# Optimization experiments

Hardware: AMD Instinct MI355X
Metric: run time of the kernel (lower is better)

## Reference

```python
import jax, jax.numpy as jnp
import numpy as np

B, S, IN, HID = 128, 512, 1024, 1024
CHI, KAPPA, DT = 0.638, 0.35, 0.01
NC = 6  # num zeta corridors


def setup_inputs() -> dict:
    key = jax.random.key(0)
    ks = jax.random.split(key, 10)
    def rn(k, shp, s=0.02):
        return jax.random.normal(k, shp, dtype=jnp.float32) * s
    return {
        "x": jax.random.normal(ks[0], (B, S, IN), dtype=jnp.float32),
        "W_gates": rn(ks[1], (IN + HID, 4 * HID)),  # fused [i|f|g|o] gate weights
        "b_gates": jnp.zeros((4 * HID,), jnp.float32),
        "mirror_W": rn(ks[2], (HID, HID)),
        "mirror_b": jnp.zeros((HID,), jnp.float32),
        "curv_W1": rn(ks[3], (HID, HID // 2)),
        "curv_b1": jnp.zeros((HID // 2,), jnp.float32),
        "curv_W2": rn(ks[4], (HID // 2, 1)),
        "curv_b2": jnp.zeros((1,), jnp.float32),
        "evo_W": rn(ks[5], (HID, HID)),
        "evo_b": jnp.zeros((HID,), jnp.float32),
        "zeta_w": jax.random.normal(ks[6], (NC,), dtype=jnp.float32),
        "zeta_p": jax.random.normal(ks[7], (NC,), dtype=jnp.float32),
    }


def _zeta_loss(zw, zp):
    # Per recurrent step seq_len==1 so s-points are (sigma=0.5, t=-2) for every batch
    # element; the functional-equation loss is therefore a single scalar independent
    # of the hidden state, and the mean over identical points equals that scalar.
    L = 0.2 + 0.1 * jnp.arange(NC, dtype=jnp.float32)  # corridor lengths
    s0 = jnp.complex64(0.5 - 2.0j)
    def xi(s):
        t1 = jnp.exp(-s * L)
        t2 = jax.nn.sigmoid(zp).astype(jnp.complex64) * jnp.exp(-(1.0 - s) * L)
        return jnp.sum(jax.nn.sigmoid(zw).astype(jnp.complex64) * 0.5 * (t1 + t2))
    d = xi(s0) - xi(1.0 - s0)
    return (d * jnp.conj(d)).real  # |Xi(s) - Xi(1-s)|^2


def reference(x, W_gates, b_gates, mirror_W, mirror_b,
              curv_W1, curv_b1, curv_W2, curv_b2,
              evo_W, evo_b, zeta_w, zeta_p):
    Wx, Wh = W_gates[:IN], W_gates[IN:]
    # Precompute the input contribution of all 4 gates for every timestep (one big GEMM).
    gx = jnp.einsum('bsi,ig->bsg', x, Wx) + b_gates        # [B,S,4H]
    gx = jnp.swapaxes(gx, 0, 1)                            # [S,B,4H] for scan
    h0 = jnp.zeros((x.shape[0], HID), x.dtype)
    c0 = jnp.zeros((x.shape[0], HID), x.dtype)

    def step(carry, g):
        h, c = carry
        gates = g + h @ Wh                                  # [B,4H]
        i, f, gg, o = jnp.split(gates, 4, axis=-1)
        i, f, o = jax.nn.sigmoid(i), jax.nn.sigmoid(f), jax.nn.sigmoid(o)
        gg = jnp.tanh(gg)
        c = f * c + i * gg
        # curvature coupling: scalar curvature per batch element gates an evolution step
        kap = CHI * (jax.nn.relu(c @ curv_W1 + curv_b1) @ curv_W2 + curv_b2)  # [B,1]
        c = c + DT * kap * (c @ evo_W + evo_b)
        # mirror operator + guardian threshold
        h = jnp.tanh((o * jnp.tanh(c)) @ mirror_W + mirror_b)
        h = h / (1.0 + KAPPA * jnp.abs(h))
        return (h, c), h

    (h, c), ys = jax.lax.scan(step, (h0, c0), gx)
    outputs = jnp.swapaxes(ys, 0, 1)                        # [B,S,H]
    # zeta regularization loss is identical each step, so the seq-mean equals one eval
    return outputs, h, c, _zeta_loss(zeta_w, zeta_p)
```

## Files before the change

### kernel.cpp

```cpp
#include <hip/hip_runtime.h>
#include <hip/hip_bf16.h>
#include <math.h>
#include <stdint.h>

#define B_    128
#define S_    512
#define IN_   1024
#define HID_  1024
#define CHI_  0.638f
#define KAPPA_ 0.35f
#define DT_   0.01f
#define CH    32
#define NCHUNK (S_/CH)

#define OUT_H 67108864
#define OUT_C 67239936
#define OUT_Z 67371008

#define WS_CNT   0
#define WS_KP    2048
#define WS_HBF   10240
#define WS_CF32  272384
#define WS_STATE_BYTES 796672
#define WS_CBF   796672
#define WS_OBF   1058816
#define WS_EBF   1320960
#define WS_WGT   1583104
#define WS_EVOT  18360320
#define WS_MIRT  20457472
#define WS_C1T   22554624
#define WS_XBF   23603200
#define WS_GXC   31991808

using s16x8 = __attribute__((ext_vector_type(8))) short;
using s16x4 = __attribute__((ext_vector_type(4))) short;
using f32x4 = __attribute__((ext_vector_type(4))) float;
typedef unsigned long long u64;

static __device__ __forceinline__ short f2bf(float x){
  unsigned int u = __float_as_uint(x);
  u = (u + 0x7FFFu + ((u >> 16) & 1u)) >> 16;
  return (short)u;
}
static __device__ __forceinline__ float b2f(short s){
  return __uint_as_float(((unsigned int)(unsigned short)s) << 16);
}
static __device__ __forceinline__ float sigf(float x){
  return 1.f / (1.f + __expf(-x));
}
static __device__ __forceinline__ float tanhf_(float x){
  return 1.f - 2.f / (__expf(2.f * x) + 1.f);
}
static __device__ __forceinline__ f32x4 mfma16(s16x8 a, s16x8 b, f32x4 c){
  return __builtin_amdgcn_mfma_f32_16x16x32_bf16(a, b, c, 0, 0, 0);
}

static __device__ __forceinline__ u64 ld_coh_u64(const void* p){
  return __hip_atomic_load((const u64*)p, __ATOMIC_RELAXED, __HIP_MEMORY_SCOPE_AGENT);
}
static __device__ __forceinline__ void st_coh_u64(void* p, u64 v){
  __hip_atomic_store((u64*)p, v, __ATOMIC_RELAXED, __HIP_MEMORY_SCOPE_AGENT);
}
static __device__ __forceinline__ float ld_coh_f32(const float* p){
  return __hip_atomic_load(p, __ATOMIC_RELAXED, __HIP_MEMORY_SCOPE_AGENT);
}
static __device__ __forceinline__ void st_coh_f32(float* p, float v){
  __hip_atomic_store(p, v, __ATOMIC_RELAXED, __HIP_MEMORY_SCOPE_AGENT);
}
static __device__ __forceinline__ unsigned ld_coh_u32(const unsigned* p){
  return __hip_atomic_load(p, __ATOMIC_RELAXED, __HIP_MEMORY_SCOPE_AGENT);
}
static __device__ __forceinline__ void st_coh_u32(unsigned* p, unsigned v){
  __hip_atomic_store(p, v, __ATOMIC_RELAXED, __HIP_MEMORY_SCOPE_AGENT);
}
static __device__ __forceinline__ void at_add_f32(float* p, float v){
  __hip_atomic_fetch_add(p, v, __ATOMIC_RELAXED, __HIP_MEMORY_SCOPE_AGENT);
}
static __device__ __forceinline__ s16x8 ld_coh16B(const short* p){
  union { u64 q[2]; s16x8 v; } u;
  u.q[0] = ld_coh_u64(p);
  u.q[1] = ld_coh_u64(p + 4);
  return u.v;
}

static __device__ __forceinline__ void gbar(unsigned* arr, int n, unsigned gen){
  asm volatile("s_waitcnt vmcnt(0)" ::: "memory");
  __syncthreads();
  if (threadIdx.x < 32){
    if (threadIdx.x == 0) st_coh_u32(arr + n, gen);
    unsigned v = ld_coh_u32(arr + threadIdx.x);
    while (!__all(v >= gen)){
      __builtin_amdgcn_s_sleep(2);
      v = ld_coh_u32(arr + threadIdx.x);
    }
  }
  __syncthreads();
}

__global__ void transpose_bf(const float* __restrict__ in, short* __restrict__ out,
                             int R, int C){
  __shared__ float tile[32][33];
  int c0 = blockIdx.x * 32, r0 = blockIdx.y * 32;
  int tc = threadIdx.x & 31, tr = threadIdx.x >> 5;
  #pragma unroll
  for (int i = 0; i < 4; i++){
    int r = tr + i * 8;
    tile[r][tc] = in[(size_t)(r0 + r) * C + (c0 + tc)];
  }
  __syncthreads();
  #pragma unroll
  for (int i = 0; i < 4; i++){
    int cc = tr + i * 8;
    out[(size_t)(c0 + cc) * R + (r0 + tc)] = f2bf(tile[tc][cc]);
  }
}

__global__ void conv_x(const float* __restrict__ x, short* __restrict__ xbf, int t0){
  int rb = blockIdx.x;
  int tl = rb >> 7, b = rb & 127;
  const float* src = x + ((size_t)b * S_ + (t0 + tl)) * (size_t)IN_;
  short* dst = xbf + (size_t)rb * IN_;
  int i = threadIdx.x * 4;
  float4 v = *(const float4*)(src + i);
  s16x4 o; o[0]=f2bf(v.x); o[1]=f2bf(v.y); o[2]=f2bf(v.z); o[3]=f2bf(v.w);
  *(s16x4*)(dst + i) = o;
}

__global__ __launch_bounds__(256, 2) void gemm_gx(const short* __restrict__ Ax,
                                                  const short* __restrict__ wgT,
                                                  short* __restrict__ gxc){
  __shared__ short As[128 * 32];
  __shared__ short Bs[128 * 32];
  const int tid = threadIdx.x, w = tid >> 6, l = tid & 63;
  const int wm = w & 1, wn = w >> 1;
  const int bn = blockIdx.x, bm = blockIdx.y;
  const int lc = l & 15, kg = l >> 4;
  f32x4 acc[4][4];
  #pragma unroll
  for (int i = 0; i < 4; i++)
    #pragma unroll
    for (int j = 0; j < 4; j++) acc[i][j] = f32x4{0.f, 0.f, 0.f, 0.f};

  const int srow = tid >> 1;
  const int so = (tid & 1) * 32;
  const short* ga = Ax  + (size_t)(bm * 128 + srow) * 1024 + (so >> 1);
  const short* gb = wgT + (size_t)(bn * 128 + srow) * 2048 + (so >> 1);
  const int sp0 = srow * 64 + ((so)      ^ ((srow & 3) << 4));
  const int sp1 = srow * 64 + ((so + 16) ^ ((srow & 3) << 4));

  uint4 ra0, ra1, rb0, rb1;
  auto LD = [&](int kt){
    ra0 = *(const uint4*)(ga + kt * 32);
    ra1 = *(const uint4*)(ga + kt * 32 + 8);
    rb0 = *(const uint4*)(gb + kt * 32);
    rb1 = *(const uint4*)(gb + kt * 32 + 8);
  };
  LD(0);
  for (int kt = 0; kt < 32; ++kt){
    __syncthreads();
    *(uint4*)((char*)As + sp0) = ra0;
    *(uint4*)((char*)As + sp1) = ra1;
    *(uint4*)((char*)Bs + sp0) = rb0;
    *(uint4*)((char*)Bs + sp1) = rb1;
    __syncthreads();
    if (kt + 1 < 32) LD(kt + 1);
    s16x8 af[4], bfr[4];
    #pragma unroll
    for (int mf = 0; mf < 4; ++mf){
      int row = wm * 64 + mf * 16 + lc;
      af[mf] = *(const s16x8*)((const char*)As + row * 64 + ((kg * 16) ^ ((row & 3) << 4)));
    }
    #pragma unroll
    for (int nf = 0; nf < 4; ++nf){
      int row = wn * 64 + nf * 16 + lc;
      bfr[nf] = *(const s16x8*)((const char*)Bs + row * 64 + ((kg * 16) ^ ((row & 3) << 4)));
    }
    #pragma unroll
    for (int mf = 0; mf < 4; ++mf)
      #pragma unroll
      for (int nf = 0; nf < 4; ++nf)
        acc[mf][nf] = mfma16(af[mf], bfr[nf], acc[mf][nf]);
  }
  #pragma unroll
  for (int mf = 0; mf < 4; ++mf){
    #pragma unroll
    for (int nf = 0; nf < 4; ++nf){
      int gg = wm * 4 + mf;
      int gc = bn * 128 + wn * 64 + nf * 16 + lc;
      s16x4 pk;
      #pragma unroll
      for (int r = 0; r < 4; r++) pk[r] = f2bf(acc[mf][nf][r]);
      *(s16x4*)(gxc + (((size_t)bm * 8 + gg) * 4096 + gc) * 16 + kg * 4) = pk;
    }
  }
}

struct cpx { double r, i; };
static __device__ cpx cexp_(cpx z){ double e = exp(z.r); return {e * cos(z.i), e * sin(z.i)}; }
static __device__ cpx xi_(double sr, double si, const float* zw, const float* zp){
  cpx acc{0.0, 0.0};
  for (int i = 0; i < 6; i++){
    double L = 0.2 + 0.1 * i;
    double sw = 1.0 / (1.0 + exp(-(double)zw[i]));
    double sp = 1.0 / (1.0 + exp(-(double)zp[i]));
    cpx t1 = cexp_({-sr * L, -si * L});
    cpx t2 = cexp_({-(1.0 - sr) * L, si * L});
    acc.r += sw * 0.5 * (t1.r + sp * t2.r);
    acc.i += sw * 0.5 * (t1.i + sp * t2.i);
  }
  return acc;
}
__global__ void zeta_k(const float* __restrict__ zw, const float* __restrict__ zp,
                       float* __restrict__ dz){
  if (threadIdx.x == 0 && blockIdx.x == 0){
    cpx a = xi_(0.5, -2.0, zw, zp);
    cpx b = xi_(0.5,  2.0, zw, zp);
    double dr = a.r - b.r, di = a.i - b.i;
    dz[0] = (float)(dr * dr + di * di);
  }
}

#define RSLOT(slot, j) ((char*)red + (slot) * 8192 + (size_t)l * 128 + (((j) * 16) ^ ((l & 7) << 4)))

__global__ __launch_bounds__(512, 2) void scan_k(
    const short* __restrict__ wgT, const short* __restrict__ evoT,
    const short* __restrict__ mirT, const short* __restrict__ c1T,
    const short* __restrict__ gxc,
    const float* __restrict__ bg,  const float* __restrict__ evob,
    const float* __restrict__ mirb, const float* __restrict__ cb1,
    const float* __restrict__ cw2, const float* __restrict__ cb2,
    short* __restrict__ hbf, short* __restrict__ cbf, short* __restrict__ obf,
    short* __restrict__ ebf, float* __restrict__ cf32, float* __restrict__ kp,
    unsigned int* __restrict__ cnt, float* __restrict__ dout, int t0)
{
  const int tid = threadIdx.x;
  const int w = tid >> 6, l = tid & 63;
  const int lc = l & 15, kg = l >> 4;
  const int bi = blockIdx.x;
  const int g = bi >> 5, n = bi & 31;
  unsigned* arr = cnt + g * 64;

  __shared__ float red[4][64][32];
  __shared__ float gatesL[4][16][33];
  __shared__ float eL[16][33];
  __shared__ float kpart[16][8];
  __shared__ float kapL[16];
  __shared__ short stL[16][32];
  __shared__ short oSt[16][32];
  __shared__ float hfL[16][32];

  const short* hG = hbf + (size_t)g * 16384;
  const short* cG = cbf + (size_t)g * 16384;
  const short* oG = obf + (size_t)g * 16384;
  const short* eG = ebf + (size_t)g * 16384;
  float* kpg = kp + g * 256;

  const int pl = (tid & 127) >> 1, ph = tid & 1;
  const size_t poff = (size_t)(n * 64 + pl) * 8 + ph * 4;
  const int psr = pl & 15, psc = (pl >> 4) * 8 + ph * 4;

  const int orow = tid >> 5, ocolL = tid & 31;
  const int ocol = n * 32 + ocolL;
  const size_t oidx = (size_t)(g * 16 + orow) * HID_ + ocol;
  float c_state = cf32[oidx];
  float bgv[4];
  #pragma unroll
  for (int q = 0; q < 4; q++) bgv[q] = bg[q * 1024 + ocol];
  const float cb2v = cb2[0];

  const short* bqp[4][2];
  #pragma unroll
  for (int q = 0; q < 4; q++)
    #pragma unroll
    for (int cf = 0; cf < 2; cf++)
      bqp[q][cf] = wgT + (size_t)(q * 1024 + n * 32 + cf * 16 + lc) * 2048 + 1024 + w * 128 + kg * 8;
  const short* bevo0 = evoT + (size_t)(n * 32 + lc) * 1024 + w * 128 + kg * 8;
  const short* bevo1 = bevo0 + 16 * 1024;
  const short* bcur  = c1T + (size_t)(n * 16 + lc) * 1024 + w * 128 + kg * 8;
  const short* bmir0 = mirT + (size_t)(n * 32 + lc) * 1024 + w * 128 + kg * 8;
  const short* bmir1 = bmir0 + 16 * 1024;
  const float eb0 = evob[n * 32 + lc], eb1 = evob[n * 32 + 16 + lc];
  const float c1bv = cb1[n * 16 + lc], c2wv = cw2[n * 16 + lc];
  const float mb0 = mirb[n * 32 + lc], mb1 = mirb[n * 32 + 16 + lc];

  unsigned gen = (unsigned)t0 * 3;

  for (int lt = 0; lt < CH; ++lt){
    const int t = t0 + lt;
    const int par = lt & 1;

    float gxv[4];
    #pragma unroll
    for (int q = 0; q < 4; q++)
      gxv[q] = b2f(gxc[(((size_t)lt * 8 + g) * 4096 + q * 1024 + ocol) * 16 + orow]);

    {
      f32x4 acc[4][2];
      #pragma unroll
      for (int q = 0; q < 4; q++){ acc[q][0] = f32x4{0,0,0,0}; acc[q][1] = f32x4{0,0,0,0}; }
      #pragma unroll
      for (int ks = 0; ks < 4; ++ks){
        int kq = w * 4 + ks;
        s16x8 a = ld_coh16B(hG + (size_t)(kq * 64 + l) * 8);
        #pragma unroll
        for (int q = 0; q < 4; q++){
          s16x8 b0 = *(const s16x8*)(bqp[q][0] + ks * 32);
          s16x8 b1 = *(const s16x8*)(bqp[q][1] + ks * 32);
          acc[q][0] = mfma16(a, b0, acc[q][0]);
          acc[q][1] = mfma16(a, b1, acc[q][1]);
        }
      }
      f32x4* accf = (f32x4*)acc;
      if (w >= 4){
        #pragma unroll
        for (int j = 0; j < 8; j++) *(f32x4*)RSLOT(w - 4, j) = accf[j];
      }
      __syncthreads();
      if (w < 4){
        #pragma unroll
        for (int j = 0; j < 8; j++) accf[j] += *(const f32x4*)RSLOT(w, j);
      }
      __syncthreads();
      if (w == 2 || w == 3){
        #pragma unroll
        for (int j = 0; j < 8; j++) *(f32x4*)RSLOT(w - 2, j) = accf[j];
      }
      __syncthreads();
      if (w < 2){
        #pragma unroll
        for (int j = 0; j < 8; j++) accf[j] += *(const f32x4*)RSLOT(w, j);
      }
      __syncthreads();
      if (w == 1){
        #pragma unroll
        for (int j = 0; j < 8; j++) *(f32x4*)RSLOT(0, j) = accf[j];
      }
      __syncthreads();
      if (w == 0){
        #pragma unroll
        for (int j = 0; j < 8; j++) accf[j] += *(const f32x4*)RSLOT(0, j);
        #pragma unroll
        for (int q = 0; q < 4; q++)
          #pragma unroll
          for (int cf = 0; cf < 2; cf++)
            #pragma unroll
            for (int r = 0; r < 4; r++)
              gatesL[q][kg * 4 + r][cf * 16 + lc] = acc[q][cf][r];
      }
      __syncthreads();
      float pre[4];
      #pragma unroll
      for (int q = 0; q < 4; q++)
        pre[q] = gatesL[q][orow][ocolL] + bgv[q] + gxv[q];
      float ii = sigf(pre[0]), ff = sigf(pre[1]);
      float gt = tanhf_(pre[2]);
      float oo = sigf(pre[3]);
      c_state = ff * c_state + ii * gt;
      stL[orow][ocolL] = f2bf(c_state);
      oSt[orow][ocolL] = f2bf(oo);
      __syncthreads();
      if (tid < 256){
        short* dst = (short*)((tid < 128 ? cG : oG) + poff);
        const short* src = (tid < 128 ? &stL[psr][psc] : &oSt[psr][psc]);
        st_coh_u64(dst, *(const u64*)src);
      }
    }
    gbar(arr, n, ++gen);

    {
      f32x4 e0{0,0,0,0}, e1{0,0,0,0}, cv{0,0,0,0};
      #pragma unroll
      for (int ks = 0; ks < 4; ++ks){
        int kq = w * 4 + ks;
        s16x8 a = ld_coh16B(cG + (size_t)(kq * 64 + l) * 8);
        s16x8 b0 = *(const s16x8*)(bevo0 + ks * 32);
        s16x8 b1 = *(const s16x8*)(bevo1 + ks * 32);
        s16x8 bc = *(const s16x8*)(bcur + ks * 32);
        e0 = mfma16(a, b0, e0);
        e1 = mfma16(a, b1, e1);
        cv = mfma16(a, bc, cv);
      }
      if (w >= 4){
        *(f32x4*)RSLOT(w - 4, 0) = e0; *(f32x4*)RSLOT(w - 4, 1) = e1; *(f32x4*)RSLOT(w - 4, 2) = cv;
      }
      __syncthreads();
      if (w < 4){
        e0 += *(const f32x4*)RSLOT(w, 0); e1 += *(const f32x4*)RSLOT(w, 1); cv += *(const f32x4*)RSLOT(w, 2);
      }
      __syncthreads();
      if (w == 2 || w == 3){
        *(f32x4*)RSLOT(w - 2, 0) = e0; *(f32x4*)RSLOT(w - 2, 1) = e1; *(f32x4*)RSLOT(w - 2, 2) = cv;
      }
      __syncthreads();
      if (w < 2){
        e0 += *(const f32x4*)RSLOT(w, 0); e1 += *(const f32x4*)RSLOT(w, 1); cv += *(const f32x4*)RSLOT(w, 2);
      }
      __syncthreads();
      if (w == 1){
        *(f32x4*)RSLOT(0, 0) = e0; *(f32x4*)RSLOT(0, 1) = e1; *(f32x4*)RSLOT(0, 2) = cv;
      }
      __syncthreads();
      if (w == 0){
        e0 += *(const f32x4*)RSLOT(0, 0); e1 += *(const f32x4*)RSLOT(0, 1); cv += *(const f32x4*)RSLOT(0, 2);
        #pragma unroll
        for (int r = 0; r < 4; r++){
          eL[kg * 4 + r][lc]      = e0[r] + eb0;
          eL[kg * 4 + r][16 + lc] = e1[r] + eb1;
          float v = fmaxf(cv[r] + c1bv, 0.f) * c2wv;
          v += __shfl_xor(v, 1); v += __shfl_xor(v, 2);
          v += __shfl_xor(v, 4); v += __shfl_xor(v, 8);
          if (lc == 0)
            at_add_f32(kpg + par * 128 + (kg * 4 + r) * 8 + (n >> 2), v);
        }
      }
      __syncthreads();
      if (tid < 128){
        union { u64 q; short s[4]; } up;
        #pragma unroll
        for (int j = 0; j < 4; j++) up.s[j] = f2bf(eL[psr][psc + j]);
        st_coh_u64((void*)(eG + poff), up.q);
      }
    }
    gbar(arr, n, ++gen);

    {
      if (tid < 128)
        kpart[tid >> 3][tid & 7] = ld_coh_f32(kpg + par * 128 + tid);
      __syncthreads();
      if (tid < 16){
        float s = 0.f;
        #pragma unroll
        for (int j = 0; j < 8; j++) s += kpart[tid][j];
        kapL[tid] = CHI_ * (s + cb2v);
      }
      __syncthreads();
      {
        float e = eL[orow][ocolL];
        c_state = c_state + DT_ * kapL[orow] * e;
        if (t == S_ - 1) dout[OUT_C + oidx] = c_state;
        if (lt == CH - 1) cf32[oidx] = c_state;
      }
      const float kap_l = kapL[lc];
      f32x4 h0{0,0,0,0}, h1{0,0,0,0};
      #pragma unroll
      for (int ks = 0; ks < 4; ++ks){
        const size_t off = (size_t)((w * 4 + ks) * 64 + l) * 8;
        s16x8 cf = ld_coh16B(cG + off);
        s16x8 ef = ld_coh16B(eG + off);
        s16x8 of = ld_coh16B(oG + off);
        s16x8 m;
        #pragma unroll
        for (int j = 0; j < 8; j++)
          m[j] = f2bf(b2f(of[j]) * tanhf_(b2f(cf[j]) + DT_ * kap_l * b2f(ef[j])));
        s16x8 b0 = *(const s16x8*)(bmir0 + ks * 32);
        s16x8 b1 = *(const s16x8*)(bmir1 + ks * 32);
        h0 = mfma16(m, b0, h0);
        h1 = mfma16(m, b1, h1);
      }
      if (w >= 4){ *(f32x4*)RSLOT(w - 4, 0) = h0; *(f32x4*)RSLOT(w - 4, 1) = h1; }
      __syncthreads();
      if (w < 4){ h0 += *(const f32x4*)RSLOT(w, 0); h1 += *(const f32x4*)RSLOT(w, 1); }
      __syncthreads();
      if (w == 2 || w == 3){ *(f32x4*)RSLOT(w - 2, 0) = h0; *(f32x4*)RSLOT(w - 2, 1) = h1; }
      __syncthreads();
      if (w < 2){ h0 += *(const f32x4*)RSLOT(w, 0); h1 += *(const f32x4*)RSLOT(w, 1); }
      __syncthreads();
      if (w == 1){ *(f32x4*)RSLOT(0, 0) = h0; *(f32x4*)RSLOT(0, 1) = h1; }
      __syncthreads();
      if (w == 0){
        h0 += *(const f32x4*)RSLOT(0, 0); h1 += *(const f32x4*)RSLOT(0, 1);
        #pragma unroll
        for (int cf = 0; cf < 2; cf++){
          #pragma unroll
          for (int r = 0; r < 4; r++){
            int row = kg * 4 + r;
            float hv = tanhf_((cf ? h1[r] : h0[r]) + (cf ? mb1 : mb0));
            hv = hv / (1.f + KAPPA_ * fabsf(hv));
            hfL[row][cf * 16 + lc] = hv;
            stL[row][cf * 16 + lc] = f2bf(hv);
          }
        }
      }
      __syncthreads();
      {
        float hv = hfL[orow][ocolL];
        dout[(size_t)(g * 16 + orow) * 524288 + (size_t)t * 1024 + ocol] = hv;
        if (t == S_ - 1) dout[OUT_H + oidx] = hv;
      }
      if (tid < 128)
        st_coh_u64((void*)(hG + poff), *(const u64*)&stL[psr][psc]);
      if (n == 0 && tid >= 128 && tid < 256)
        st_coh_f32(kpg + (par ^ 1) * 128 + (tid - 128), 0.f);
    }
    gbar(arr, n, ++gen);
  }
}

extern "C" void kernel_launch(void* const* d_in, const int* in_sizes, int n_in,
                              void* d_out, int out_size, void* d_ws, size_t ws_size,
                              hipStream_t stream)
{
  (void)in_sizes; (void)n_in; (void)out_size; (void)ws_size;
  const float* x   = (const float*)d_in[0];
  const float* Wg  = (const float*)d_in[1];
  const float* bg  = (const float*)d_in[2];
  const float* miW = (const float*)d_in[3];
  const float* mib = (const float*)d_in[4];
  const float* c1W = (const float*)d_in[5];
  const float* c1b = (const float*)d_in[6];
  const float* c2W = (const float*)d_in[7];
  const float* c2b = (const float*)d_in[8];
  const float* evW = (const float*)d_in[9];
  const float* evb = (const float*)d_in[10];
  const float* zw  = (const float*)d_in[11];
  const float* zp  = (const float*)d_in[12];
  float* out = (float*)d_out;
  char* ws = (char*)d_ws;

  unsigned int* cnt = (unsigned int*)(ws + WS_CNT);
  float* kpb  = (float*)(ws + WS_KP);
  short* hbf  = (short*)(ws + WS_HBF);
  float* cf32 = (float*)(ws + WS_CF32);
  short* cbf  = (short*)(ws + WS_CBF);
  short* obf  = (short*)(ws + WS_OBF);
  short* ebf  = (short*)(ws + WS_EBF);
  short* wgT  = (short*)(ws + WS_WGT);
  short* evoT = (short*)(ws + WS_EVOT);
  short* mirT = (short*)(ws + WS_MIRT);
  short* c1T  = (short*)(ws + WS_C1T);
  short* xbf  = (short*)(ws + WS_XBF);
  short* gxc  = (short*)(ws + WS_GXC);

  hipMemsetAsync(ws, 0, WS_STATE_BYTES, stream);

  transpose_bf<<<dim3(4096/32, 2048/32), 256, 0, stream>>>(Wg,  wgT, 2048, 4096);
  transpose_bf<<<dim3(1024/32, 1024/32), 256, 0, stream>>>(evW, evoT, 1024, 1024);
  transpose_bf<<<dim3(1024/32, 1024/32), 256, 0, stream>>>(miW, mirT, 1024, 1024);
  transpose_bf<<<dim3(512/32, 1024/32),  256, 0, stream>>>(c1W, c1T, 1024, 512);

  zeta_k<<<1, 64, 0, stream>>>(zw, zp, out + OUT_Z);

  for (int ch = 0; ch < NCHUNK; ++ch){
    conv_x<<<dim3(CH * 128), 256, 0, stream>>>(x, xbf, ch * CH);
    gemm_gx<<<dim3(32, CH), 256, 0, stream>>>(xbf, wgT, gxc);
    scan_k<<<dim3(256), 512, 0, stream>>>(wgT, evoT, mirT, c1T, gxc,
                                          bg, evb, mib, c1b, c2W, c2b,
                                          hbf, cbf, obf, ebf, cf32, kpb,
                                          cnt, out, ch * CH);
  }
}
```

Measured before the change: 12.63 ms.

## Linearize mirror input via tanh first-order expansion to split kappa from GEMM

```diff
diff --git a/kernel.cpp b/kernel.cpp
--- a/kernel.cpp
+++ b/kernel.cpp
@@ -23,8 +23,8 @@
 #define WS_CF32  272384
 #define WS_STATE_BYTES 796672
 #define WS_CBF   796672
-#define WS_OBF   1058816
-#define WS_EBF   1320960
+#define WS_M0    1058816
+#define WS_M1    1320960
 #define WS_WGT   1583104
 #define WS_EVOT  18360320
 #define WS_MIRT  20457472
@@ -229,8 +229,8 @@
     const float* __restrict__ bg,  const float* __restrict__ evob,
     const float* __restrict__ mirb, const float* __restrict__ cb1,
     const float* __restrict__ cw2, const float* __restrict__ cb2,
-    short* __restrict__ hbf, short* __restrict__ cbf, short* __restrict__ obf,
-    short* __restrict__ ebf, float* __restrict__ cf32, float* __restrict__ kp,
+    short* __restrict__ hbf, short* __restrict__ cbf, short* __restrict__ m0bf,
+    short* __restrict__ m1bf, float* __restrict__ cf32, float* __restrict__ kp,
     unsigned int* __restrict__ cnt, float* __restrict__ dout, int t0)
 {
   const int tid = threadIdx.x;
@@ -246,13 +246,13 @@
   __shared__ float kpart[16][8];
   __shared__ float kapL[16];
   __shared__ short stL[16][32];
-  __shared__ short oSt[16][32];
+  __shared__ short m0St[16][32];
   __shared__ float hfL[16][32];
 
-  const short* hG = hbf + (size_t)g * 16384;
-  const short* cG = cbf + (size_t)g * 16384;
-  const short* oG = obf + (size_t)g * 16384;
-  const short* eG = ebf + (size_t)g * 16384;
+  const short* hG  = hbf  + (size_t)g * 16384;
+  const short* cG  = cbf  + (size_t)g * 16384;
+  const short* m0G = m0bf + (size_t)g * 16384;
+  const short* m1G = m1bf + (size_t)g * 16384;
   float* kpg = kp + g * 256;
 
   const int pl = (tid & 127) >> 1, ph = tid & 1;
@@ -263,6 +263,7 @@
   const int ocol = n * 32 + ocolL;
   const size_t oidx = (size_t)(g * 16 + orow) * HID_ + ocol;
   float c_state = cf32[oidx];
+  float o_reg = 0.f, th_reg = 0.f;
   float bgv[4];
   #pragma unroll
   for (int q = 0; q < 4; q++) bgv[q] = bg[q * 1024 + ocol];
@@ -354,14 +355,15 @@
         pre[q] = gatesL[q][orow][ocolL] + bgv[q] + gxv[q];
       float ii = sigf(pre[0]), ff = sigf(pre[1]);
       float gt = tanhf_(pre[2]);
-      float oo = sigf(pre[3]);
+      o_reg = sigf(pre[3]);
       c_state = ff * c_state + ii * gt;
-      stL[orow][ocolL] = f2bf(c_state);
-      oSt[orow][ocolL] = f2bf(oo);
+      th_reg = tanhf_(c_state);
+      stL[orow][ocolL]  = f2bf(c_state);
+      m0St[orow][ocolL] = f2bf(o_reg * th_reg);
       __syncthreads();
       if (tid < 256){
-        short* dst = (short*)((tid < 128 ? cG : oG) + poff);
-        const short* src = (tid < 128 ? &stL[psr][psc] : &oSt[psr][psc]);
+        short* dst = (short*)((tid < 128 ? cG : m0G) + poff);
+        const short* src = (tid < 128 ? &stL[psr][psc] : &m0St[psr][psc]);
         st_coh_u64(dst, *(const u64*)src);
       }
     }
@@ -414,12 +416,14 @@
         }
       }
       __syncthreads();
-      if (tid < 128){
-        union { u64 q; short s[4]; } up;
-        #pragma unroll
-        for (int j = 0; j < 4; j++) up.s[j] = f2bf(eL[psr][psc + j]);
-        st_coh_u64((void*)(eG + poff), up.q);
-      }
+      {
+        float e = eL[orow][ocolL];
+        float m1 = o_reg * e * (1.f - th_reg * th_reg);
+        stL[orow][ocolL] = f2bf(m1);
+      }
+      __syncthreads();
+      if (tid < 128)
+        st_coh_u64((void*)(m1G + poff), *(const u64*)&stL[psr][psc]);
     }
     gbar(arr, n, ++gen);
 
@@ -440,41 +444,56 @@
         if (t == S_ - 1) dout[OUT_C + oidx] = c_state;
         if (lt == CH - 1) cf32[oidx] = c_state;
       }
-      const float kap_l = kapL[lc];
-      f32x4 h0{0,0,0,0}, h1{0,0,0,0};
+      f32x4 hh[4];
+      #pragma unroll
+      for (int j = 0; j < 4; j++) hh[j] = f32x4{0,0,0,0};
       #pragma unroll
       for (int ks = 0; ks < 4; ++ks){
         const size_t off = (size_t)((w * 4 + ks) * 64 + l) * 8;
-        s16x8 cf = ld_coh16B(cG + off);
-        s16x8 ef = ld_coh16B(eG + off);
-        s16x8 of = ld_coh16B(oG + off);
-        s16x8 m;
-        #pragma unroll
-        for (int j = 0; j < 8; j++)
-          m[j] = f2bf(b2f(of[j]) * tanhf_(b2f(cf[j]) + DT_ * kap_l * b2f(ef[j])));
+        s16x8 a0 = ld_coh16B(m0G + off);
+        s16x8 a1 = ld_coh16B(m1G + off);
         s16x8 b0 = *(const s16x8*)(bmir0 + ks * 32);
         s16x8 b1 = *(const s16x8*)(bmir1 + ks * 32);
-        h0 = mfma16(m, b0, h0);
-        h1 = mfma16(m, b1, h1);
-      }
-      if (w >= 4){ *(f32x4*)RSLOT(w - 4, 0) = h0; *(f32x4*)RSLOT(w - 4, 1) = h1; }
-      __syncthreads();
-      if (w < 4){ h0 += *(const f32x4*)RSLOT(w, 0); h1 += *(const f32x4*)RSLOT(w, 1); }
-      __syncthreads();
-      if (w == 2 || w == 3){ *(f32x4*)RSLOT(w - 2, 0) = h0; *(f32x4*)RSLOT(w - 2, 1) = h1; }
-      __syncthreads();
-      if (w < 2){ h0 += *(const f32x4*)RSLOT(w, 0); h1 += *(const f32x4*)RSLOT(w, 1); }
-      __syncthreads();
-      if (w == 1){ *(f32x4*)RSLOT(0, 0) = h0; *(f32x4*)RSLOT(0, 1) = h1; }
+        hh[0] = mfma16(a0, b0, hh[0]);
+        hh[1] = mfma16(a0, b1, hh[1]);
+        hh[2] = mfma16(a1, b0, hh[2]);
+        hh[3] = mfma16(a1, b1, hh[3]);
+      }
+      if (w >= 4){
+        #pragma unroll
+        for (int j = 0; j < 4; j++) *(f32x4*)RSLOT(w - 4, j) = hh[j];
+      }
+      __syncthreads();
+      if (w < 4){
+        #pragma unroll
+        for (int j = 0; j < 4; j++) hh[j] += *(const f32x4*)RSLOT(w, j);
+      }
+      __syncthreads();
+      if (w == 2 || w == 3){
+        #pragma unroll
+        for (int j = 0; j < 4; j++) *(f32x4*)RSLOT(w - 2, j) = hh[j];
+      }
+      __syncthreads();
+      if (w < 2){
+        #pragma unroll
+        for (int j = 0; j < 4; j++) hh[j] += *(const f32x4*)RSLOT(w, j);
+      }
+      __syncthreads();
+      if (w == 1){
+        #pragma unroll
+        for (int j = 0; j < 4; j++) *(f32x4*)RSLOT(0, j) = hh[j];
+      }
       __syncthreads();
       if (w == 0){
-        h0 += *(const f32x4*)RSLOT(0, 0); h1 += *(const f32x4*)RSLOT(0, 1);
+        #pragma unroll
+        for (int j = 0; j < 4; j++) hh[j] += *(const f32x4*)RSLOT(0, j);
         #pragma unroll
         for (int cf = 0; cf < 2; cf++){
           #pragma unroll
           for (int r = 0; r < 4; r++){
             int row = kg * 4 + r;
-            float hv = tanhf_((cf ? h1[r] : h0[r]) + (cf ? mb1 : mb0));
+            float hp = hh[cf][r] + DT_ * kapL[row] * hh[2 + cf][r] + (cf ? mb1 : mb0);
+            float hv = tanhf_(hp);
             hv = hv / (1.f + KAPPA_ * fabsf(hv));
             hfL[row][cf * 16 + lc] = hv;
             stL[row][cf * 16 + lc] = f2bf(hv);
@@ -522,8 +541,8 @@
   short* hbf  = (short*)(ws + WS_HBF);
   float* cf32 = (float*)(ws + WS_CF32);
   short* cbf  = (short*)(ws + WS_CBF);
-  short* obf  = (short*)(ws + WS_OBF);
-  short* ebf  = (short*)(ws + WS_EBF);
+  short* m0bf = (short*)(ws + WS_M0);
+  short* m1bf = (short*)(ws + WS_M1);
   short* wgT  = (short*)(ws + WS_WGT);
   short* evoT = (short*)(ws + WS_EVOT);
   short* mirT = (short*)(ws + WS_MIRT);
@@ -545,7 +564,7 @@
     gemm_gx<<<dim3(32, CH), 256, 0, stream>>>(xbf, wgT, gxc);
     scan_k<<<dim3(256), 512, 0, stream>>>(wgT, evoT, mirT, c1T, gxc,
                                           bg, evb, mib, c1b, c2W, c2b,
-                                          hbf, cbf, obf, ebf, cf32, kpb,
+                                          hbf, cbf, m0bf, m1bf, cf32, kpb,
                                           cnt, out, ch * CH);
   }
 }
```

Measured after the change: 13.14 ms. 1.04x slower.
